# Optimization experiments

Hardware: AMD Instinct MI355X
Metric: run time of the kernel (lower is better)

Reference implementation:

```python
import jax, jax.numpy as jnp
import numpy as np

B, T, I, H = 512, 128, 128, 512


def setup_inputs() -> dict:
    key = jax.random.key(0)
    ks = jax.random.split(key, 10)
    scale = 1.0 / np.sqrt(I + H)
    return {
        "s_inputs": jax.random.normal(ks[0], (B, T, I), jnp.float32),
        "l_inputs": jax.random.normal(ks[1], (B, T, I), jnp.float32),
        "dow": jax.random.randint(ks[2], (B,), 0, 7),
        "hour": jax.random.randint(ks[3], (B,), 0, 24),
        # gate weights stacked as [f, i, o, C] along output dim (math-equivalent
        # to 4 separate nn.Linear(input_size+hidden_size, hidden_size))
        "s_W": jax.random.uniform(ks[4], (I + H, 4 * H), jnp.float32, -scale, scale),
        "s_b": jax.random.uniform(ks[5], (4 * H,), jnp.float32, -scale, scale),
        "l_W": jax.random.uniform(ks[6], (I + H, 4 * H), jnp.float32, -scale, scale),
        "l_b": jax.random.uniform(ks[7], (4 * H,), jnp.float32, -scale, scale),
        "out_W": jax.random.uniform(ks[8], (2 * H, H), jnp.float32, -1.0 / np.sqrt(2 * H), 1.0 / np.sqrt(2 * H)),
        "out_b": jax.random.uniform(ks[9], (H,), jnp.float32, -1.0 / np.sqrt(2 * H), 1.0 / np.sqrt(2 * H)),
    }


def _cell(x, h, c, W, b):
    # one LSTM step: fused 4-gate GEMM then elementwise gate math
    g = jnp.concatenate([x, h], axis=1) @ W + b  # [B, 4H]
    f, i, o, cand = jnp.split(g, 4, axis=1)
    c_new = jax.nn.sigmoid(f) * c + jax.nn.sigmoid(i) * jnp.tanh(cand)
    h_new = jax.nn.sigmoid(o) * jnp.tanh(c_new)
    return h_new, c_new


def reference(s_inputs, l_inputs, dow, hour, s_W, s_b, l_W, l_b, out_W, out_b):
    batch = s_inputs.shape[0]
    hdim = out_b.shape[0]
    init = (jnp.zeros((batch, hdim), s_inputs.dtype),) * 4  # (sh, sc, lh, lc)

    def step(carry, xs):
        sh, sc, lh, lc = carry
        x_s, x_l = xs
        sh, sc = _cell(x_s, sh, sc, s_W, s_b)
        lh, lc = _cell(x_l, lh, lc, l_W, l_b)
        return (sh, sc, lh, lc), None

    xs = (jnp.swapaxes(s_inputs, 0, 1), jnp.swapaxes(l_inputs, 0, 1))  # [T,B,I]
    (sh, _, lh, _), _ = jax.lax.scan(step, init, xs)
    return jnp.tanh(jnp.concatenate([sh, lh], axis=1) @ out_W + out_b)
```

## Files before the change

### kernel.cpp

```cpp
#include <hip/hip_runtime.h>

#define HD 512
#define KD 640
#define G4 2048

typedef short short8 __attribute__((ext_vector_type(8)));
typedef __bf16 bf16x8 __attribute__((ext_vector_type(8)));
typedef float floatx4 __attribute__((ext_vector_type(4)));
typedef unsigned int uintx4 __attribute__((ext_vector_type(4)));

static __device__ __forceinline__ unsigned short f2bf(float f) {
  unsigned int u = __float_as_uint(f);
  u += 0x7fffu + ((u >> 16) & 1u);
  return (unsigned short)(u >> 16);
}
static __device__ __forceinline__ float rcp_(float x) {
  return __builtin_amdgcn_rcpf(x);
}
static __device__ __forceinline__ float sigmoidf_(float x) {
  return rcp_(1.f + __expf(-x));
}
static __device__ __forceinline__ float tanhf_(float x) {
  float ax = fabsf(x);
  float e = __expf(-2.f * ax);
  float r = fmaf(-2.f * e, rcp_(1.f + e), 1.f);
  return copysignf(r, x);
}
static __device__ __forceinline__ void store16_cc(unsigned long long a, uintx4 v) {
  asm volatile("global_store_dwordx4 %0, %1, off sc0 sc1" :: "v"(a), "v"(v) : "memory");
}
static __device__ __forceinline__ void waitcnt_vm0() {
  asm volatile("s_waitcnt vmcnt(0)" ::: "memory");
}
static __device__ __forceinline__ void load_lds16_cc(const void* g, void* l) {
  __builtin_amdgcn_global_load_lds(
      (const __attribute__((address_space(1))) void*)(unsigned long long)(uintptr_t)g,
      (__attribute__((address_space(3))) void*)l, 16, 0, 17);
}

__global__ __launch_bounds__(256) void transpose_f32_bf16(
    const float* __restrict__ src, unsigned short* __restrict__ dst,
    int R, int C) {
  __shared__ unsigned short tile[64][80];
  int nR = R >> 6;
  int tr = blockIdx.x % nR;
  int tc = blockIdx.x / nR;
  int tid = threadIdx.x;
#pragma unroll
  for (int i = 0; i < 2; ++i) {
    int seg = tid + i * 256;
    int row = seg >> 3, ks8 = (seg & 7) * 8;
    const float* p = src + (size_t)(tr * 64 + row) * C + tc * 64 + ks8;
    short8 v;
#pragma unroll
    for (int q = 0; q < 8; ++q) v[q] = (short)f2bf(p[q]);
    *(short8*)(&tile[row][ks8]) = v;
  }
  __syncthreads();
#pragma unroll
  for (int i = 0; i < 2; ++i) {
    int seg = tid + i * 256;
    int cl = seg >> 3, rs8 = (seg & 7) * 8;
    short8 v;
#pragma unroll
    for (int q = 0; q < 8; ++q) v[q] = (short)tile[rs8 + q][cl];
    *(short8*)(dst + (size_t)(tc * 64 + cl) * R + tr * 64 + rs8) = v;
  }
}

__global__ __launch_bounds__(256) void xconv(
    const float* __restrict__ xs, const float* __restrict__ xl,
    unsigned short* __restrict__ xTs, unsigned short* __restrict__ xTl) {
  int t = blockIdx.x & 127;
  int bc = (blockIdx.x >> 7) & 3;
  int which = blockIdx.x >> 9;
  const float* x = which ? xl : xs;
  unsigned short* xT = which ? xTl : xTs;
  int b0 = bc * 128;
#pragma unroll
  for (int i = 0; i < 8; ++i) {
    int seg = threadIdx.x + i * 256;
    int bl_ = seg >> 4, i8 = (seg & 15) * 8;
    const float* p = x + (size_t)(b0 + bl_) * 16384 + t * 128 + i8;
    short8 v;
#pragma unroll
    for (int q = 0; q < 8; ++q) v[q] = (short)f2bf(p[q]);
    *(short8*)(xT + ((size_t)t * 512 + b0 + bl_) * 128 + i8) = v;
  }
}

__global__ __launch_bounds__(256, 1) void lstm_persistent(
    const unsigned short* __restrict__ xTs, const unsigned short* __restrict__ xTl,
    const unsigned short* __restrict__ WTs, const unsigned short* __restrict__ WTl,
    const float* __restrict__ bs, const float* __restrict__ bl,
    unsigned short* __restrict__ hs0, unsigned short* __restrict__ hs1,
    unsigned short* __restrict__ hl0, unsigned short* __restrict__ hl1,
    int* __restrict__ flags) {
  const int bid = blockIdx.x;
  const int lstm = bid & 1;
  const int mb = (bid >> 1) & 15;
  const int nb = bid >> 5;
  const int grp = lstm * 16 + mb;
  const int b0 = mb * 32;
  const int H0 = nb * 64;

  const unsigned short* xT = lstm ? xTl : xTs;
  const unsigned short* WT = lstm ? WTl : WTs;
  const float* bias = lstm ? bl : bs;
  unsigned short* h0 = lstm ? hl0 : hs0;
  unsigned short* h1 = lstm ? hl1 : hs1;

  __shared__ unsigned short As[32][648];
  __shared__ unsigned short hbw[4][32][24];

  const int tid = threadIdx.x;
  const int wn = tid >> 6;
  const int lane = tid & 63;
  const int quad = lane >> 4;
  const int lrow = lane & 15;
  const int colL = wn * 16 + lrow;

  if (tid == 0) {
    unsigned xcc;
    asm("s_getreg_b32 %0, hwreg(20, 0, 32)" : "=s"(xcc));
    __hip_atomic_store(flags + 1024 + bid, (int)(xcc & 255u) + 1,
                       __ATOMIC_RELAXED, __HIP_MEMORY_SCOPE_AGENT);
  }

  float bias_r[4];
#pragma unroll
  for (int g = 0; g < 4; ++g) bias_r[g] = bias[g * HD + H0 + colL];
  float c_r[8];
#pragma unroll
  for (int j = 0; j < 8; ++j) c_r[j] = 0.f;

  bf16x8 breg[4][20];
#pragma unroll
  for (int g = 0; g < 4; ++g) {
    const unsigned short* wp = WT + (size_t)(g * HD + H0 + colL) * KD + quad * 8;
#pragma unroll
    for (int kc = 0; kc < 20; ++kc)
      breg[g][kc] = __builtin_bit_cast(bf16x8, *(const short8*)(wp + kc * 32));
  }

  const int srow = lane >> 1, sc8 = (lane & 1) * 8;
  const unsigned long long hstA =
      (unsigned long long)(h1 + (size_t)(b0 + srow) * HD + H0 + wn * 16 + sc8);
  const unsigned long long hstB =
      (unsigned long long)(h0 + (size_t)(b0 + srow) * HD + H0 + wn * 16 + sc8);

#pragma unroll
  for (int i = 0; i < 2; ++i) {
    int seg = tid + i * 256;
    int row = seg >> 4, ch = seg & 15;
    short8 v = *(const short8*)(xT + ((size_t)(b0 + row)) * 128 + ch * 8);
    *(short8*)(&As[row][ch * 8]) = v;
  }
#pragma unroll
  for (int i = 0; i < 8; ++i) {
    int chunk = tid + i * 256;
    int row = chunk >> 6, ch = chunk & 63;
    *(uintx4*)(&As[row][128 + ch * 8]) = (uintx4){0, 0, 0, 0};
  }

#pragma unroll 1
  for (int t = 0; t < 128; ++t) {
    const unsigned short* hr = (t & 1) ? h1 : h0;

    if (t > 0 && wn == 0) {
      while (true) {
        int v = __hip_atomic_load(flags + grp * 32 + (lane & 7),
                                  __ATOMIC_RELAXED, __HIP_MEMORY_SCOPE_AGENT);
        if (__ballot(v >= t) == 0xFFFFFFFFFFFFFFFFull) break;
        __builtin_amdgcn_s_sleep(1);
      }
    }
    __syncthreads();

    if (t > 0) {
#pragma unroll
      for (int i = 0; i < 8; ++i) {
        int row = wn + i * 4;
        load_lds16_cc(hr + (size_t)(b0 + row) * HD + lane * 8, &As[row][128]);
      }
    }

    floatx4 acc[2][4];
#pragma unroll
    for (int mt = 0; mt < 2; ++mt)
#pragma unroll
      for (int g = 0; g < 4; ++g) acc[mt][g] = (floatx4){0.f, 0.f, 0.f, 0.f};
#pragma unroll
    for (int kc = 0; kc < 4; ++kc) {
      bf16x8 a0 = __builtin_bit_cast(bf16x8, *(const short8*)(&As[lrow][kc * 32 + quad * 8]));
      bf16x8 a1 = __builtin_bit_cast(bf16x8, *(const short8*)(&As[16 + lrow][kc * 32 + quad * 8]));
#pragma unroll
      for (int g = 0; g < 4; ++g) {
        acc[0][g] = __builtin_amdgcn_mfma_f32_16x16x32_bf16(a0, breg[g][kc], acc[0][g], 0, 0, 0);
        acc[1][g] = __builtin_amdgcn_mfma_f32_16x16x32_bf16(a1, breg[g][kc], acc[1][g], 0, 0, 0);
      }
    }

    waitcnt_vm0();
    __syncthreads();

    short8 xv[2];
#pragma unroll
    for (int i = 0; i < 2; ++i) {
      int seg = tid + i * 256;
      int row = seg >> 4, ch = seg & 15;
      xv[i] = *(const short8*)(xT + ((size_t)(t + 1) * 512 + b0 + row) * 128 + ch * 8);
    }

#pragma unroll
    for (int kc = 4; kc < 20; ++kc) {
      bf16x8 a0 = __builtin_bit_cast(bf16x8, *(const short8*)(&As[lrow][kc * 32 + quad * 8]));
      bf16x8 a1 = __builtin_bit_cast(bf16x8, *(const short8*)(&As[16 + lrow][kc * 32 + quad * 8]));
#pragma unroll
      for (int g = 0; g < 4; ++g) {
        acc[0][g] = __builtin_amdgcn_mfma_f32_16x16x32_bf16(a0, breg[g][kc], acc[0][g], 0, 0, 0);
        acc[1][g] = __builtin_amdgcn_mfma_f32_16x16x32_bf16(a1, breg[g][kc], acc[1][g], 0, 0, 0);
      }
    }

#pragma unroll
    for (int mt = 0; mt < 2; ++mt)
#pragma unroll
      for (int r = 0; r < 4; ++r) {
        int j = mt * 4 + r;
        float fg = acc[mt][0][r] + bias_r[0];
        float ig = acc[mt][1][r] + bias_r[1];
        float og = acc[mt][2][r] + bias_r[2];
        float cg = acc[mt][3][r] + bias_r[3];
        float cn = sigmoidf_(fg) * c_r[j] + sigmoidf_(ig) * tanhf_(cg);
        float hn = sigmoidf_(og) * tanhf_(cn);
        c_r[j] = cn;
        hbw[wn][mt * 16 + quad * 4 + r][lrow] = f2bf(hn);
      }
    asm volatile("s_waitcnt lgkmcnt(0)" ::: "memory");
    short8 hv8 = *(const short8*)(&hbw[wn][srow][sc8]);

    store16_cc((t & 1) ? hstB : hstA, __builtin_bit_cast(uintx4, hv8));

    waitcnt_vm0();
    if (t < 127 && tid == 0)
      __hip_atomic_store(flags + grp * 32 + nb, t + 1,
                         __ATOMIC_RELAXED, __HIP_MEMORY_SCOPE_AGENT);

    if (t < 127) {
#pragma unroll
      for (int i = 0; i < 2; ++i) {
        int seg = tid + i * 256;
        int row = seg >> 4, ch = seg & 15;
        *(short8*)(&As[row][ch * 8]) = xv[i];
      }
    }
  }
}

__global__ __launch_bounds__(256) void out_gemm(
    const unsigned short* __restrict__ hs, const unsigned short* __restrict__ hl,
    const unsigned short* __restrict__ WTo,
    const float* __restrict__ ob, float* __restrict__ out) {
  const int bx = blockIdx.x;
  const int mb = bx & 7;
  const int nb = bx >> 3;

  __shared__ unsigned short As2[64][88];
  __shared__ unsigned short Bs2[128][88];

  const int tid = threadIdx.x;
  const int wave = tid >> 6;
  const int lane = tid & 63;
  const int quad = lane >> 4;
  const int lrow = lane & 15;
  const int wm = wave & 1;
  const int wn = wave >> 1;

  floatx4 acc[8];
#pragma unroll
  for (int i = 0; i < 8; ++i) acc[i] = (floatx4){0.f, 0.f, 0.f, 0.f};

  for (int k0 = 0; k0 < 1024; k0 += 64) {
#pragma unroll
    for (int i = 0; i < 2; ++i) {
      int seg = tid + i * 256;
      int row = seg >> 3, ks8 = (seg & 7) * 8;
      int kg = k0 + ks8;
      int b = mb * 64 + row;
      const unsigned short* src =
          (kg < 512) ? (hs + (size_t)b * HD + kg) : (hl + (size_t)b * HD + (kg - 512));
      *(short8*)(&As2[row][ks8]) = *(const short8*)src;
    }
#pragma unroll
    for (int i = 0; i < 4; ++i) {
      int seg = tid + i * 256;
      int n = seg >> 3, ks8 = (seg & 7) * 8;
      *(short8*)(&Bs2[n][ks8]) =
          *(const short8*)(WTo + (size_t)(nb * 128 + n) * 1024 + k0 + ks8);
    }
    __syncthreads();
#pragma unroll
    for (int ks = 0; ks < 64; ks += 32) {
      int kq = ks + quad * 8;
      bf16x8 a0 = __builtin_bit_cast(bf16x8, *(const short8*)(&As2[wm * 32 + lrow][kq]));
      bf16x8 a1 = __builtin_bit_cast(bf16x8, *(const short8*)(&As2[wm * 32 + 16 + lrow][kq]));
#pragma unroll
      for (int nt = 0; nt < 4; ++nt) {
        bf16x8 bfr = __builtin_bit_cast(bf16x8, *(const short8*)(&Bs2[wn * 64 + nt * 16 + lrow][kq]));
        acc[nt] = __builtin_amdgcn_mfma_f32_16x16x32_bf16(a0, bfr, acc[nt], 0, 0, 0);
        acc[4 + nt] = __builtin_amdgcn_mfma_f32_16x16x32_bf16(a1, bfr, acc[4 + nt], 0, 0, 0);
      }
    }
    __syncthreads();
  }
#pragma unroll
  for (int mt = 0; mt < 2; ++mt) {
#pragma unroll
    for (int nt = 0; nt < 4; ++nt) {
      int n = nb * 128 + wn * 64 + nt * 16 + lrow;
      float bv = ob[n];
#pragma unroll
      for (int r = 0; r < 4; ++r) {
        int b = mb * 64 + wm * 32 + mt * 16 + quad * 4 + r;
        out[(size_t)b * HD + n] = tanhf_(acc[mt * 4 + nt][r] + bv);
      }
    }
  }
}

extern "C" void kernel_launch(void* const* d_in, const int* in_sizes, int n_in,
                              void* d_out, int out_size, void* d_ws, size_t ws_size,
                              hipStream_t stream) {
  (void)in_sizes; (void)n_in; (void)out_size; (void)ws_size;
  const float* xs = (const float*)d_in[0];
  const float* xl = (const float*)d_in[1];
  const float* sW = (const float*)d_in[4];
  const float* sb = (const float*)d_in[5];
  const float* lW = (const float*)d_in[6];
  const float* lb = (const float*)d_in[7];
  const float* oW = (const float*)d_in[8];
  const float* ob = (const float*)d_in[9];

  char* w = (char*)d_ws;
  int* flags = (int*)w;
  unsigned short* WTs = (unsigned short*)(w + 8192);
  unsigned short* WTl = WTs + (size_t)G4 * KD;
  unsigned short* WTo = WTl + (size_t)G4 * KD;
  unsigned short* xTs = WTo + (size_t)HD * 1024;
  unsigned short* xTl = xTs + (size_t)128 * 512 * 128;
  unsigned short* hs0 = xTl + (size_t)128 * 512 * 128;
  unsigned short* hs1 = hs0 + (size_t)512 * HD;
  unsigned short* hl0 = hs1 + (size_t)512 * HD;
  unsigned short* hl1 = hl0 + (size_t)512 * HD;

  hipMemsetAsync(flags, 0, 8192, stream);
  transpose_f32_bf16<<<(640 / 64) * (2048 / 64), 256, 0, stream>>>(sW, WTs, 640, 2048);
  transpose_f32_bf16<<<(640 / 64) * (2048 / 64), 256, 0, stream>>>(lW, WTl, 640, 2048);
  transpose_f32_bf16<<<(1024 / 64) * (512 / 64), 256, 0, stream>>>(oW, WTo, 1024, 512);
  xconv<<<1024, 256, 0, stream>>>(xs, xl, xTs, xTl);

  const float* sbp = sb; const float* lbp = lb;
  const unsigned short *xTs_c = xTs, *xTl_c = xTl, *WTs_c = WTs, *WTl_c = WTl;
  unsigned short *a_hs0 = hs0, *a_hs1 = hs1, *a_hl0 = hl0, *a_hl1 = hl1;
  int* a_flags = flags;
  void* args[] = {(void*)&xTs_c, (void*)&xTl_c, (void*)&WTs_c, (void*)&WTl_c,
                  (void*)&sbp, (void*)&lbp, (void*)&a_hs0, (void*)&a_hs1,
                  (void*)&a_hl0, (void*)&a_hl1, (void*)&a_flags};
  hipError_t e = hipLaunchCooperativeKernel((const void*)lstm_persistent,
                                            dim3(256), dim3(256), args, 0, stream);
  if (e != hipSuccess) {
    lstm_persistent<<<256, 256, 0, stream>>>(xTs, xTl, WTs, WTl, sb, lb,
                                             hs0, hs1, hl0, hl1, flags);
  }
  out_gemm<<<32, 256, 0, stream>>>(hs0, hl0, WTo, ob, (float*)d_out);
}
```

Before: 716.9 us.

## Double-buffer LSTM recurrent operands in LDS and split h-load wait per row half

Splits the shared A tile into double-buffered x and h buffers indexed by step parity. This removes the top-of-loop block barrier, makes every wave poll the flags itself, and prefetches x two steps ahead into registers. The h-part GEMM is split so rows 0-15 start after a partial vmcnt(4) wait while the second half of the h loads lands, overlapping global-to-LDS transfer with MFMA work. The cost is more LDS, more flag polling traffic from all waves, and fragile reliance on exact vmcnt ordering of outstanding loads.

```diff
diff --git a/kernel.cpp b/kernel.cpp
--- a/kernel.cpp
+++ b/kernel.cpp
@@ -31,6 +31,12 @@
 }
 static __device__ __forceinline__ void waitcnt_vm0() {
   asm volatile("s_waitcnt vmcnt(0)" ::: "memory");
+}
+static __device__ __forceinline__ void waitcnt_vm4() {
+  asm volatile("s_waitcnt vmcnt(4)" ::: "memory");
+}
+static __device__ __forceinline__ void waitcnt_lgkm0() {
+  asm volatile("s_waitcnt lgkmcnt(0)" ::: "memory");
 }
 static __device__ __forceinline__ void load_lds16_cc(const void* g, void* l) {
   __builtin_amdgcn_global_load_lds(
@@ -110,7 +116,8 @@
   unsigned short* h0 = lstm ? hl0 : hs0;
   unsigned short* h1 = lstm ? hl1 : hs1;
 
-  __shared__ unsigned short As[32][648];
+  __shared__ unsigned short Ah[2][32][520];
+  __shared__ unsigned short Ax[2][32][128];
   __shared__ unsigned short hbw[4][32][24];
 
   const int tid = threadIdx.x;
@@ -154,34 +161,38 @@
     int seg = tid + i * 256;
     int row = seg >> 4, ch = seg & 15;
     short8 v = *(const short8*)(xT + ((size_t)(b0 + row)) * 128 + ch * 8);
-    *(short8*)(&As[row][ch * 8]) = v;
+    *(short8*)(&Ax[0][row][ch * 8]) = v;
   }
 #pragma unroll
   for (int i = 0; i < 8; ++i) {
     int chunk = tid + i * 256;
     int row = chunk >> 6, ch = chunk & 63;
-    *(uintx4*)(&As[row][128 + ch * 8]) = (uintx4){0, 0, 0, 0};
-  }
+    *(uintx4*)(&Ah[0][row][ch * 8]) = (uintx4){0, 0, 0, 0};
+  }
+  short8 xv[2];
+#pragma unroll
+  for (int i = 0; i < 2; ++i) {
+    int seg = tid + i * 256;
+    int row = seg >> 4, ch = seg & 15;
+    xv[i] = *(const short8*)(xT + ((size_t)512 + b0 + row) * 128 + ch * 8);
+  }
+  __syncthreads();
 
 #pragma unroll 1
   for (int t = 0; t < 128; ++t) {
     const unsigned short* hr = (t & 1) ? h1 : h0;
 
-    if (t > 0 && wn == 0) {
+    if (t > 0) {
       while (true) {
         int v = __hip_atomic_load(flags + grp * 32 + (lane & 7),
                                   __ATOMIC_RELAXED, __HIP_MEMORY_SCOPE_AGENT);
         if (__ballot(v >= t) == 0xFFFFFFFFFFFFFFFFull) break;
         __builtin_amdgcn_s_sleep(1);
       }
-    }
-    __syncthreads();
-
-    if (t > 0) {
 #pragma unroll
       for (int i = 0; i < 8; ++i) {
         int row = wn + i * 4;
-        load_lds16_cc(hr + (size_t)(b0 + row) * HD + lane * 8, &As[row][128]);
+        load_lds16_cc(hr + (size_t)(b0 + row) * HD + lane * 8, &Ah[t & 1][row][0]);
       }
     }
 
@@ -192,8 +203,8 @@
       for (int g = 0; g < 4; ++g) acc[mt][g] = (floatx4){0.f, 0.f, 0.f, 0.f};
 #pragma unroll
     for (int kc = 0; kc < 4; ++kc) {
-      bf16x8 a0 = __builtin_bit_cast(bf16x8, *(const short8*)(&As[lrow][kc * 32 + quad * 8]));
-      bf16x8 a1 = __builtin_bit_cast(bf16x8, *(const short8*)(&As[16 + lrow][kc * 32 + quad * 8]));
+      bf16x8 a0 = __builtin_bit_cast(bf16x8, *(const short8*)(&Ax[t & 1][lrow][kc * 32 + quad * 8]));
+      bf16x8 a1 = __builtin_bit_cast(bf16x8, *(const short8*)(&Ax[t & 1][16 + lrow][kc * 32 + quad * 8]));
 #pragma unroll
       for (int g = 0; g < 4; ++g) {
         acc[0][g] = __builtin_amdgcn_mfma_f32_16x16x32_bf16(a0, breg[g][kc], acc[0][g], 0, 0, 0);
@@ -201,26 +212,38 @@
       }
     }
 
+    waitcnt_vm4();
+
+    if (t < 127) {
+#pragma unroll
+      for (int i = 0; i < 2; ++i) {
+        int seg = tid + i * 256;
+        int row = seg >> 4, ch = seg & 15;
+        *(short8*)(&Ax[(t + 1) & 1][row][ch * 8]) = xv[i];
+      }
+    }
+    waitcnt_lgkm0();
+    __builtin_amdgcn_s_barrier();
+    __builtin_amdgcn_sched_barrier(0);
+
+#pragma unroll
+    for (int kc = 4; kc < 20; ++kc) {
+      bf16x8 a0 = __builtin_bit_cast(bf16x8, *(const short8*)(&Ah[t & 1][lrow][(kc - 4) * 32 + quad * 8]));
+#pragma unroll
+      for (int g = 0; g < 4; ++g)
+        acc[0][g] = __builtin_amdgcn_mfma_f32_16x16x32_bf16(a0, breg[g][kc], acc[0][g], 0, 0, 0);
+    }
+
     waitcnt_vm0();
-    __syncthreads();
-
-    short8 xv[2];
-#pragma unroll
-    for (int i = 0; i < 2; ++i) {
-      int seg = tid + i * 256;
-      int row = seg >> 4, ch = seg & 15;
-      xv[i] = *(const short8*)(xT + ((size_t)(t + 1) * 512 + b0 + row) * 128 + ch * 8);
-    }
+    __builtin_amdgcn_s_barrier();
+    __builtin_amdgcn_sched_barrier(0);
 
 #pragma unroll
     for (int kc = 4; kc < 20; ++kc) {
-      bf16x8 a0 = __builtin_bit_cast(bf16x8, *(const short8*)(&As[lrow][kc * 32 + quad * 8]));
-      bf16x8 a1 = __builtin_bit_cast(bf16x8, *(const short8*)(&As[16 + lrow][kc * 32 + quad * 8]));
-#pragma unroll
-      for (int g = 0; g < 4; ++g) {
-        acc[0][g] = __builtin_amdgcn_mfma_f32_16x16x32_bf16(a0, breg[g][kc], acc[0][g], 0, 0, 0);
+      bf16x8 a1 = __builtin_bit_cast(bf16x8, *(const short8*)(&Ah[t & 1][16 + lrow][(kc - 4) * 32 + quad * 8]));
+#pragma unroll
+      for (int g = 0; g < 4; ++g)
         acc[1][g] = __builtin_amdgcn_mfma_f32_16x16x32_bf16(a1, breg[g][kc], acc[1][g], 0, 0, 0);
-      }
     }
 
 #pragma unroll
@@ -237,7 +260,7 @@
         c_r[j] = cn;
         hbw[wn][mt * 16 + quad * 4 + r][lrow] = f2bf(hn);
       }
-    asm volatile("s_waitcnt lgkmcnt(0)" ::: "memory");
+    waitcnt_lgkm0();
     short8 hv8 = *(const short8*)(&hbw[wn][srow][sc8]);
 
     store16_cc((t & 1) ? hstB : hstA, __builtin_bit_cast(uintx4, hv8));
@@ -247,12 +270,12 @@
       __hip_atomic_store(flags + grp * 32 + nb, t + 1,
                          __ATOMIC_RELAXED, __HIP_MEMORY_SCOPE_AGENT);
 
-    if (t < 127) {
+    if (t < 126) {
 #pragma unroll
       for (int i = 0; i < 2; ++i) {
         int seg = tid + i * 256;
         int row = seg >> 4, ch = seg & 15;
-        *(short8*)(&As[row][ch * 8]) = xv[i];
+        xv[i] = *(const short8*)(xT + ((size_t)(t + 2) * 512 + b0 + row) * 128 + ch * 8);
       }
     }
   }
```

Result: slower. 842.1 us (+17.5%).

## Split persistent LSTM across 512 blocks with 16-row batch tiles

Applied to the files above, without the earlier changes.

Doubles the persistent grid from 256 to 512 blocks by halving each block's batch tile from 32 to 16 rows, so each block does half the MFMA work per step. Launch bounds change to allow two blocks per CU, and the flag groups are re-indexed to 32 per LSTM. The long-LSTM blocks also sleep briefly at startup to stagger them against the short-LSTM blocks, and the XCC-id diagnostic store is removed. This cuts per-step latency on the serial recurrence, but it doubles the register-resident weight copies and the synchronization traffic, and two blocks per CU must fit the large breg register footprint.

```diff
diff --git a/kernel.cpp b/kernel.cpp
--- a/kernel.cpp
+++ b/kernel.cpp
@@ -89,7 +89,7 @@
   }
 }
 
-__global__ __launch_bounds__(256, 1) void lstm_persistent(
+__global__ __launch_bounds__(256, 2) void lstm_persistent(
     const unsigned short* __restrict__ xTs, const unsigned short* __restrict__ xTl,
     const unsigned short* __restrict__ WTs, const unsigned short* __restrict__ WTl,
     const float* __restrict__ bs, const float* __restrict__ bl,
@@ -98,10 +98,10 @@
     int* __restrict__ flags) {
   const int bid = blockIdx.x;
   const int lstm = bid & 1;
-  const int mb = (bid >> 1) & 15;
-  const int nb = bid >> 5;
-  const int grp = lstm * 16 + mb;
-  const int b0 = mb * 32;
+  const int mb = (bid >> 1) & 31;
+  const int nb = bid >> 6;
+  const int grp = lstm * 32 + mb;
+  const int b0 = mb * 16;
   const int H0 = nb * 64;
 
   const unsigned short* xT = lstm ? xTl : xTs;
@@ -110,8 +110,8 @@
   unsigned short* h0 = lstm ? hl0 : hs0;
   unsigned short* h1 = lstm ? hl1 : hs1;
 
-  __shared__ unsigned short As[32][648];
-  __shared__ unsigned short hbw[4][32][24];
+  __shared__ unsigned short As[16][648];
+  __shared__ unsigned short hbw[4][16][24];
 
   const int tid = threadIdx.x;
   const int wn = tid >> 6;
@@ -120,19 +120,12 @@
   const int lrow = lane & 15;
   const int colL = wn * 16 + lrow;
 
-  if (tid == 0) {
-    unsigned xcc;
-    asm("s_getreg_b32 %0, hwreg(20, 0, 32)" : "=s"(xcc));
-    __hip_atomic_store(flags + 1024 + bid, (int)(xcc & 255u) + 1,
-                       __ATOMIC_RELAXED, __HIP_MEMORY_SCOPE_AGENT);
-  }
-
   float bias_r[4];
 #pragma unroll
   for (int g = 0; g < 4; ++g) bias_r[g] = bias[g * HD + H0 + colL];
-  float c_r[8];
-#pragma unroll
-  for (int j = 0; j < 8; ++j) c_r[j] = 0.f;
+  float c_r[4];
+#pragma unroll
+  for (int j = 0; j < 4; ++j) c_r[j] = 0.f;
 
   bf16x8 breg[4][20];
 #pragma unroll
@@ -149,18 +142,23 @@
   const unsigned long long hstB =
       (unsigned long long)(h0 + (size_t)(b0 + srow) * HD + H0 + wn * 16 + sc8);
 
-#pragma unroll
-  for (int i = 0; i < 2; ++i) {
-    int seg = tid + i * 256;
-    int row = seg >> 4, ch = seg & 15;
+  {
+    int row = tid >> 4, ch = tid & 15;
     short8 v = *(const short8*)(xT + ((size_t)(b0 + row)) * 128 + ch * 8);
     *(short8*)(&As[row][ch * 8]) = v;
   }
 #pragma unroll
-  for (int i = 0; i < 8; ++i) {
+  for (int i = 0; i < 4; ++i) {
     int chunk = tid + i * 256;
     int row = chunk >> 6, ch = chunk & 63;
     *(uintx4*)(&As[row][128 + ch * 8]) = (uintx4){0, 0, 0, 0};
+  }
+  __syncthreads();
+
+  if (lstm) {
+    __builtin_amdgcn_s_sleep(15);
+    __builtin_amdgcn_s_sleep(15);
+    __builtin_amdgcn_s_sleep(15);
   }
 
 #pragma unroll 1
@@ -179,68 +177,57 @@
 
     if (t > 0) {
 #pragma unroll
-      for (int i = 0; i < 8; ++i) {
+      for (int i = 0; i < 4; ++i) {
         int row = wn + i * 4;
         load_lds16_cc(hr + (size_t)(b0 + row) * HD + lane * 8, &As[row][128]);
       }
     }
 
-    floatx4 acc[2][4];
-#pragma unroll
-    for (int mt = 0; mt < 2; ++mt)
-#pragma unroll
-      for (int g = 0; g < 4; ++g) acc[mt][g] = (floatx4){0.f, 0.f, 0.f, 0.f};
+    floatx4 acc[4];
+#pragma unroll
+    for (int g = 0; g < 4; ++g) acc[g] = (floatx4){0.f, 0.f, 0.f, 0.f};
 #pragma unroll
     for (int kc = 0; kc < 4; ++kc) {
       bf16x8 a0 = __builtin_bit_cast(bf16x8, *(const short8*)(&As[lrow][kc * 32 + quad * 8]));
-      bf16x8 a1 = __builtin_bit_cast(bf16x8, *(const short8*)(&As[16 + lrow][kc * 32 + quad * 8]));
-#pragma unroll
-      for (int g = 0; g < 4; ++g) {
-        acc[0][g] = __builtin_amdgcn_mfma_f32_16x16x32_bf16(a0, breg[g][kc], acc[0][g], 0, 0, 0);
-        acc[1][g] = __builtin_amdgcn_mfma_f32_16x16x32_bf16(a1, breg[g][kc], acc[1][g], 0, 0, 0);
-      }
+#pragma unroll
+      for (int g = 0; g < 4; ++g)
+        acc[g] = __builtin_amdgcn_mfma_f32_16x16x32_bf16(a0, breg[g][kc], acc[g], 0, 0, 0);
     }
 
     waitcnt_vm0();
     __syncthreads();
 
-    short8 xv[2];
-#pragma unroll
-    for (int i = 0; i < 2; ++i) {
-      int seg = tid + i * 256;
-      int row = seg >> 4, ch = seg & 15;
-      xv[i] = *(const short8*)(xT + ((size_t)(t + 1) * 512 + b0 + row) * 128 + ch * 8);
+    short8 xv;
+    if (t < 127) {
+      int row = tid >> 4, ch = tid & 15;
+      xv = *(const short8*)(xT + ((size_t)(t + 1) * 512 + b0 + row) * 128 + ch * 8);
     }
 
 #pragma unroll
     for (int kc = 4; kc < 20; ++kc) {
       bf16x8 a0 = __builtin_bit_cast(bf16x8, *(const short8*)(&As[lrow][kc * 32 + quad * 8]));
-      bf16x8 a1 = __builtin_bit_cast(bf16x8, *(const short8*)(&As[16 + lrow][kc * 32 + quad * 8]));
-#pragma unroll
-      for (int g = 0; g < 4; ++g) {
-        acc[0][g] = __builtin_amdgcn_mfma_f32_16x16x32_bf16(a0, breg[g][kc], acc[0][g], 0, 0, 0);
-        acc[1][g] = __builtin_amdgcn_mfma_f32_16x16x32_bf16(a1, breg[g][kc], acc[1][g], 0, 0, 0);
-      }
-    }
-
-#pragma unroll
-    for (int mt = 0; mt < 2; ++mt)
-#pragma unroll
-      for (int r = 0; r < 4; ++r) {
-        int j = mt * 4 + r;
-        float fg = acc[mt][0][r] + bias_r[0];
-        float ig = acc[mt][1][r] + bias_r[1];
-        float og = acc[mt][2][r] + bias_r[2];
-        float cg = acc[mt][3][r] + bias_r[3];
-        float cn = sigmoidf_(fg) * c_r[j] + sigmoidf_(ig) * tanhf_(cg);
-        float hn = sigmoidf_(og) * tanhf_(cn);
-        c_r[j] = cn;
-        hbw[wn][mt * 16 + quad * 4 + r][lrow] = f2bf(hn);
-      }
+#pragma unroll
+      for (int g = 0; g < 4; ++g)
+        acc[g] = __builtin_amdgcn_mfma_f32_16x16x32_bf16(a0, breg[g][kc], acc[g], 0, 0, 0);
+    }
+
+#pragma unroll
+    for (int r = 0; r < 4; ++r) {
+      float fg = acc[0][r] + bias_r[0];
+      float ig = acc[1][r] + bias_r[1];
+      float og = acc[2][r] + bias_r[2];
+      float cg = acc[3][r] + bias_r[3];
+      float cn = sigmoidf_(fg) * c_r[r] + sigmoidf_(ig) * tanhf_(cg);
+      float hn = sigmoidf_(og) * tanhf_(cn);
+      c_r[r] = cn;
+      hbw[wn][quad * 4 + r][lrow] = f2bf(hn);
+    }
     asm volatile("s_waitcnt lgkmcnt(0)" ::: "memory");
-    short8 hv8 = *(const short8*)(&hbw[wn][srow][sc8]);
-
-    store16_cc((t & 1) ? hstB : hstA, __builtin_bit_cast(uintx4, hv8));
+
+    if (lane < 32) {
+      short8 hv8 = *(const short8*)(&hbw[wn][srow][sc8]);
+      store16_cc((t & 1) ? hstB : hstA, __builtin_bit_cast(uintx4, hv8));
+    }
 
     waitcnt_vm0();
     if (t < 127 && tid == 0)
@@ -248,12 +235,8 @@
                          __ATOMIC_RELAXED, __HIP_MEMORY_SCOPE_AGENT);
 
     if (t < 127) {
-#pragma unroll
-      for (int i = 0; i < 2; ++i) {
-        int seg = tid + i * 256;
-        int row = seg >> 4, ch = seg & 15;
-        *(short8*)(&As[row][ch * 8]) = xv[i];
-      }
+      int row = tid >> 4, ch = tid & 15;
+      *(short8*)(&As[row][ch * 8]) = xv;
     }
   }
 }
@@ -368,9 +351,9 @@
                   (void*)&sbp, (void*)&lbp, (void*)&a_hs0, (void*)&a_hs1,
                   (void*)&a_hl0, (void*)&a_hl1, (void*)&a_flags};
   hipError_t e = hipLaunchCooperativeKernel((const void*)lstm_persistent,
-                                            dim3(256), dim3(256), args, 0, stream);
+                                            dim3(512), dim3(256), args, 0, stream);
   if (e != hipSuccess) {
-    lstm_persistent<<<256, 256, 0, stream>>>(xTs, xTl, WTs, WTl, sb, lb,
+    lstm_persistent<<<512, 256, 0, stream>>>(xTs, xTl, WTs, WTl, sb, lb,
                                              hs0, hs1, hl0, hl1, flags);
   }
   out_gemm<<<32, 256, 0, stream>>>(hs0, hl0, WTo, ob, (float*)d_out);
```

Result: slower. 2.185 ms (+204.9%).
